# Kernel tuning notes

Measured on AMD Instinct MI355X. Metric: run time of the kernel, lower is better.

Reference implementation:

```python
import math
import jax, jax.numpy as jnp
import numpy as np

B, S, D, H, FF, N, V, C = 32, 512, 512, 8, 2048, 6, 32000, 16
EPS = 1e-6


def setup_inputs() -> dict:
    key = jax.random.key(0)
    c = [0]
    def w(shape, scale=0.02):
        c[0] += 1
        return jax.random.normal(jax.random.fold_in(key, c[0]), shape, jnp.float32) * scale
    inp = {}
    inp['src_emb'] = w((V, D)).at[0].set(0.0)  # padding_idx=0 row zeroed
    inp['tgt_emb'] = w((C, D)).at[0].set(0.0)
    for p in ['e', 'd', 's']:  # encoder self / decoder self / decoder cross attn
        for nm in ['wq', 'wk', 'wv', 'wo']:
            inp[f'{p}_{nm}'] = w((N, D, D))
            inp[f'{p}_{nm.replace("w", "b")}'] = w((N, D))
    for p in ['e', 'd']:
        inp[f'{p}_w1'] = w((N, D, FF)); inp[f'{p}_b1'] = w((N, FF))
        inp[f'{p}_w2'] = w((N, FF, D)); inp[f'{p}_b2'] = w((N, D))
    inp['gen_w'] = w((D * C, C)); inp['gen_b'] = w((C,))
    inp['scr_x'] = jax.random.randint(jax.random.fold_in(key, 999), (B, S), 0, V, dtype=jnp.int32)
    return inp


def _layernorm(x):
    # torch source: (x - mean) / (std + eps), std is unbiased (ddof=1); gamma=1, beta=0
    m = x.mean(-1, keepdims=True)
    s = jnp.std(x, axis=-1, keepdims=True, ddof=1)
    return (x - m) / (s + EPS)


def _mha(xq, xkv, wq, bq, wk, bk, wv, bv, wo, bo):
    b, lq, _ = xq.shape
    lk = xkv.shape[1]
    dk = D // H
    q = (xq @ wq + bq).reshape(b, lq, H, dk)
    k = (xkv @ wk + bk).reshape(b, lk, H, dk)
    v = (xkv @ wv + bv).reshape(b, lk, H, dk)
    scores = jnp.einsum('bqhd,bkhd->bhqk', q, k) / math.sqrt(dk)
    p = jax.nn.softmax(scores, axis=-1)
    o = jnp.einsum('bhqk,bkhd->bqhd', p, v).reshape(b, lq, D)
    return o @ wo + bo


def _ffn(x, w1, b1, w2, b2):
    return jax.nn.relu(x @ w1 + b1) @ w2 + b2


def _pos_encoding(L):
    pos = jnp.arange(L, dtype=jnp.float32)[:, None]
    div = jnp.exp(jnp.arange(0, D, 2, dtype=jnp.float32) * (-math.log(10000.0) / D))
    pe = jnp.zeros((L, D), jnp.float32)
    pe = pe.at[:, 0::2].set(jnp.sin(pos * div))
    pe = pe.at[:, 1::2].set(jnp.cos(pos * div))
    return pe


def reference(src_emb, tgt_emb,
              e_wq, e_bq, e_wk, e_bk, e_wv, e_bv, e_wo, e_bo, e_w1, e_b1, e_w2, e_b2,
              d_wq, d_bq, d_wk, d_bk, d_wv, d_bv, d_wo, d_bo,
              s_wq, s_bq, s_wk, s_bk, s_wv, s_bv, s_wo, s_bo,
              d_w1, d_b1, d_w2, d_b2, gen_w, gen_b, scr_x):
    sqrt_d = math.sqrt(D)
    # encoder
    x = src_emb[scr_x] * sqrt_d + _pos_encoding(S)[None]
    for i in range(N):
        t = _layernorm(x)
        x = x + _mha(t, t, e_wq[i], e_bq[i], e_wk[i], e_bk[i], e_wv[i], e_bv[i], e_wo[i], e_bo[i])
        t = _layernorm(x)
        x = x + _ffn(t, e_w1[i], e_b1[i], e_w2[i], e_b2[i])
    enc = _layernorm(x)
    # decoder over classify targets arange(C), repeated over batch
    y = jnp.broadcast_to(tgt_emb * sqrt_d + _pos_encoding(C), (B, C, D))
    for i in range(N):
        t = _layernorm(y)
        y = y + _mha(t, t, d_wq[i], d_bq[i], d_wk[i], d_bk[i], d_wv[i], d_bv[i], d_wo[i], d_bo[i])
        t = _layernorm(y)
        y = y + _mha(t, enc, s_wq[i], s_bq[i], s_wk[i], s_bk[i], s_wv[i], s_bv[i], s_wo[i], s_bo[i])
        t = _layernorm(y)
        y = y + _ffn(t, d_w1[i], d_b1[i], d_w2[i], d_b2[i])
    dec = _layernorm(y)
    logits = dec.reshape(B, -1) @ gen_w + gen_b
    return jax.nn.log_softmax(logits, axis=-1)
```

## Files before the change

kernel.cpp:

```cpp
#include <hip/hip_runtime.h>
#include <math.h>

#define NB  32
#define SS  512
#define DD  512
#define HH  8
#define FFD 2048
#define NLAY 6
#define CC  16
#define SQRTD 22.627416997969522f

typedef unsigned short u16;
typedef __attribute__((ext_vector_type(8))) short short8;
typedef __attribute__((ext_vector_type(8))) unsigned short u16x8;
typedef __attribute__((ext_vector_type(4))) float f32x4;

__device__ __forceinline__ u16 f2bf(float f) {
  unsigned u = __builtin_bit_cast(unsigned, f);
  u += 0x7fff + ((u >> 16) & 1);
  return (u16)(u >> 16);
}
__device__ __forceinline__ float bf2f(u16 u) {
  unsigned v = ((unsigned)u) << 16;
  return __builtin_bit_cast(float, v);
}
__device__ __forceinline__ void async16(const u16* g, u16* l) {
  __builtin_amdgcn_global_load_lds(
      (const __attribute__((address_space(1))) unsigned int*)g,
      (__attribute__((address_space(3))) unsigned int*)l, 16, 0, 0);
}
__device__ __forceinline__ int swz(int row, int slice) {
  return row * 128 + ((slice ^ (row & 7)) << 4);
}
__device__ __forceinline__ int vswz(int row, int slice) {
  return row * 128 + ((slice ^ (row & 7) ^ ((row >> 4) & 3)) << 4);
}

__device__ __forceinline__ float pe_val(int pos, int d) {
  int j = d >> 1;
  float freq = expf((float)j * -0.03597789207f);
  float ang = (float)pos * freq;
  return (d & 1) ? cosf(ang) : sinf(ang);
}

__global__ __launch_bounds__(512) void k_embed_src(
    const float* __restrict__ emb, const int* __restrict__ ids,
    float* __restrict__ x) {
  int tok = blockIdx.x;
  int d = threadIdx.x;
  int s = tok & (SS - 1);
  int id = ids[tok];
  x[(size_t)tok * DD + d] = emb[(size_t)id * DD + d] * SQRTD + pe_val(s, d);
}

__global__ __launch_bounds__(512) void k_embed_tgt(
    const float* __restrict__ emb, float* __restrict__ y) {
  int tok = blockIdx.x;
  int d = threadIdx.x;
  int c = tok & (CC - 1);
  y[(size_t)tok * DD + d] = emb[(size_t)c * DD + d] * SQRTD + pe_val(c, d);
}

template <typename OT>
__global__ __launch_bounds__(256) void k_layernorm(
    const float* __restrict__ X, OT* __restrict__ Y) {
  int row = blockIdx.x;
  int tid = threadIdx.x;
  int lane = tid & 63, wv = tid >> 6;
  const float* x = X + (size_t)row * DD;
  float2 v = *(const float2*)(x + tid * 2);
  float s = v.x + v.y;
  #pragma unroll
  for (int off = 32; off; off >>= 1) s += __shfl_xor(s, off);
  __shared__ float red[4];
  if (lane == 0) red[wv] = s;
  __syncthreads();
  float mean = (red[0] + red[1] + red[2] + red[3]) * (1.0f / DD);
  float dx = v.x - mean, dy = v.y - mean;
  float sq = dx * dx + dy * dy;
  #pragma unroll
  for (int off = 32; off; off >>= 1) sq += __shfl_xor(sq, off);
  __syncthreads();
  if (lane == 0) red[wv] = sq;
  __syncthreads();
  float var = (red[0] + red[1] + red[2] + red[3]) * (1.0f / (DD - 1));
  float inv = 1.0f / (sqrtf(var) + 1e-6f);
  float ox = dx * inv, oy = dy * inv;
  if constexpr (sizeof(OT) == 2) {
    ushort2 o; o.x = f2bf(ox); o.y = f2bf(oy);
    *(ushort2*)((u16*)Y + (size_t)row * DD + tid * 2) = o;
  } else {
    float2 o; o.x = ox; o.y = oy;
    *(float2*)((float*)Y + (size_t)row * DD + tid * 2) = o;
  }
}

__global__ __launch_bounds__(256) void k_wt(
    const float* __restrict__ in, u16* __restrict__ out, int K, int N,
    size_t ldl, int roff) {
  __shared__ float tile[32][33];
  const float* ip = in + (size_t)blockIdx.z * K * N;
  u16* op = out + (size_t)blockIdx.z * ldl;
  int n0 = blockIdx.x * 32, k0 = blockIdx.y * 32;
  int tx = threadIdx.x, ty = threadIdx.y;
  #pragma unroll
  for (int i = 0; i < 32; i += 8)
    tile[ty + i][tx] = ip[(size_t)(k0 + ty + i) * N + n0 + tx];
  __syncthreads();
  #pragma unroll
  for (int i = 0; i < 32; i += 8)
    op[(size_t)(roff + n0 + ty + i) * K + k0 + tx] = f2bf(tile[tx][ty + i]);
}

__global__ void k_bcat(const float* __restrict__ b0, const float* __restrict__ b1,
                       const float* __restrict__ b2, float* __restrict__ out,
                       int n0, int n1, int n2) {
  int lay = blockIdx.x, nt = n0 + n1 + n2;
  for (int t = threadIdx.x; t < nt; t += blockDim.x) {
    float v;
    if (t < n0) v = b0[(size_t)lay * n0 + t];
    else if (t < n0 + n1) v = b1[(size_t)lay * n1 + t - n0];
    else v = b2[(size_t)lay * n2 + t - n0 - n1];
    out[(size_t)lay * nt + t] = v;
  }
}

template <typename OT, bool RELU, bool RES, int NT>
__global__ __launch_bounds__(256) void k_mgemm(
    const u16* __restrict__ A, const u16* __restrict__ Bt,
    const float* __restrict__ bias, const float* __restrict__ res,
    OT* __restrict__ C, int M, int N, int K) {
  constexpr int MI = (NT == 128) ? 4 : 2;
  __shared__ u16 As[2][128 * 32];
  __shared__ u16 Bs[2][NT * 32];
  int nbn = N / NT;
  int cpx = gridDim.x >> 3;
  int bid = (blockIdx.x & 7) * cpx + (blockIdx.x >> 3);
  int bm = bid / nbn, bn = bid % nbn;
  int tid = threadIdx.x;
  int wid = tid >> 6, lane = tid & 63;
  int i0 = 2 * wid, i1 = 2 * wid + 1;
  int r0 = 16 * i0 + (lane >> 2), r1 = 16 * i1 + (lane >> 2);
  int kof = (lane & 3) * 8;
  const u16* Ag0 = A + (size_t)(bm * 128 + r0) * K + kof;
  const u16* Ag1 = A + (size_t)(bm * 128 + r1) * K + kof;
  const u16* Bg0;
  const u16* Bg1 = nullptr;
  if constexpr (NT == 128) {
    Bg0 = Bt + (size_t)(bn * 128 + r0) * K + kof;
    Bg1 = Bt + (size_t)(bn * 128 + r1) * K + kof;
  } else {
    int rb = 16 * wid + (lane >> 2);
    Bg0 = Bt + (size_t)(bn * 64 + rb) * K + kof;
  }
  f32x4 acc[MI][4] = {};
  int wm = wid >> 1, wn = wid & 1;
  int aoff, boff;
  if constexpr (NT == 128) {
    aoff = (wm * 64 + (lane & 15)) * 32 + (lane >> 4) * 8;
    boff = (wn * 64 + (lane & 15)) * 32 + (lane >> 4) * 8;
  } else {
    aoff = (wid * 32 + (lane & 15)) * 32 + (lane >> 4) * 8;
    boff = (lane & 15) * 32 + (lane >> 4) * 8;
  }

  auto stage = [&](int buf, int kel) {
    async16(Ag0 + kel, &As[buf][i0 * 512]);
    async16(Ag1 + kel, &As[buf][i1 * 512]);
    if constexpr (NT == 128) {
      async16(Bg0 + kel, &Bs[buf][i0 * 512]);
      async16(Bg1 + kel, &Bs[buf][i1 * 512]);
    } else {
      async16(Bg0 + kel, &Bs[buf][wid * 512]);
    }
  };

  stage(0, 0);
  __syncthreads();
  int nkt = K >> 5;
  for (int kt = 0; kt < nkt; ++kt) {
    int cur = kt & 1;
    if (kt + 1 < nkt) stage(cur ^ 1, (kt + 1) << 5);
    short8 af[MI], bfr[4];
    #pragma unroll
    for (int i = 0; i < MI; ++i)
      af[i] = *(const short8*)&As[cur][aoff + i * 16 * 32];
    #pragma unroll
    for (int i = 0; i < 4; ++i)
      bfr[i] = *(const short8*)&Bs[cur][boff + i * 16 * 32];
    #pragma unroll
    for (int mi = 0; mi < MI; ++mi)
      #pragma unroll
      for (int ni = 0; ni < 4; ++ni)
        acc[mi][ni] = __builtin_amdgcn_mfma_f32_16x16x32_bf16(
            af[mi], bfr[ni], acc[mi][ni], 0, 0, 0);
    __syncthreads();
  }

  int colb, rowb;
  if constexpr (NT == 128) {
    colb = bn * 128 + wn * 64 + (lane & 15);
    rowb = bm * 128 + wm * 64 + ((lane >> 4) << 2);
  } else {
    colb = bn * 64 + (lane & 15);
    rowb = bm * 128 + wid * 32 + ((lane >> 4) << 2);
  }
  #pragma unroll
  for (int mi = 0; mi < MI; ++mi)
    #pragma unroll
    for (int ni = 0; ni < 4; ++ni) {
      int col = colb + ni * 16;
      float bv = bias[col];
      #pragma unroll
      for (int r = 0; r < 4; ++r) {
        int row = rowb + mi * 16 + r;
        float v = acc[mi][ni][r] + bv;
        if constexpr (RES) v += res[(size_t)row * N + col];
        if constexpr (RELU) v = fmaxf(v, 0.f);
        if constexpr (sizeof(OT) == 2) ((u16*)C)[(size_t)row * N + col] = f2bf(v);
        else ((float*)C)[(size_t)row * N + col] = v;
      }
    }
}

__global__ __launch_bounds__(256) void k_attn3(
    const u16* __restrict__ Q, const u16* __restrict__ K,
    const u16* __restrict__ V, u16* __restrict__ O,
    int Lq, int Lk, int nqt, int ldq, int ldk, int ldv, int ldo) {
  __shared__ u16 Qs[64 * 64];
  __shared__ u16 Ks[64 * 64];
  __shared__ u16 VsT[64 * 64];
  __shared__ u16 Ps[64 * 64];
  int cpx = gridDim.x >> 3;
  int bid = (blockIdx.x & 7) * cpx + (blockIdx.x >> 3);
  int qt = bid % nqt;
  int bh = bid / nqt;
  int b = bh >> 3, h = bh & 7;
  int tid = threadIdx.x;
  int wv = tid >> 6, lane = tid & 63;
  int l16 = lane & 15, l4 = lane >> 4;
  int sr = tid >> 2;
  int sc2 = (tid & 3) << 1;

  {
    int qr = qt * 64 + sr;
    const u16* g = Q + (size_t)((size_t)b * Lq + qr) * ldq + h * 64 + (sc2 << 3);
    u16x8 v0 = *(const u16x8*)g;
    u16x8 v1 = *(const u16x8*)(g + 8);
    *(u16x8*)((char*)Qs + swz(sr, sc2)) = v0;
    *(u16x8*)((char*)Qs + swz(sr, sc2 + 1)) = v1;
  }

  f32x4 o_acc[4] = {};
  float l_r[4] = {0.f, 0.f, 0.f, 0.f};
  int qrow = wv * 16 + l16;

  int nkt = Lk >> 6;
  for (int kt = 0; kt < nkt; ++kt) {
    __syncthreads();
    {
      int kr = kt * 64 + sr;
      const u16* gk = K + (size_t)((size_t)b * Lk + kr) * ldk + h * 64 + (sc2 << 3);
      const u16* gv = V + (size_t)((size_t)b * Lk + kr) * ldv + h * 64 + (sc2 << 3);
      u16x8 k0 = *(const u16x8*)gk;
      u16x8 k1 = *(const u16x8*)(gk + 8);
      u16x8 vv0 = *(const u16x8*)gv;
      u16x8 vv1 = *(const u16x8*)(gv + 8);
      *(u16x8*)((char*)Ks + swz(sr, sc2)) = k0;
      *(u16x8*)((char*)Ks + swz(sr, sc2 + 1)) = k1;
      bool oddr = sr & 1;
      u16x8 send = oddr ? vv0 : vv1;
      int4 si = __builtin_bit_cast(int4, send);
      int4 ri;
      ri.x = __shfl_xor(si.x, 4); ri.y = __shfl_xor(si.y, 4);
      ri.z = __shfl_xor(si.z, 4); ri.w = __shfl_xor(si.w, 4);
      u16x8 recv = __builtin_bit_cast(u16x8, ri);
      int colbyte = (sr & 6) << 1;
      int slice = sr >> 3;
      int dbase = (sc2 << 3) + (oddr ? 8 : 0);
      #pragma unroll
      for (int j = 0; j < 8; ++j) {
        u16 lo = oddr ? recv[j] : vv0[j];
        u16 hi = oddr ? vv1[j] : recv[j];
        *(unsigned*)((char*)VsT + vswz(dbase + j, slice) + colbyte) =
            (unsigned)lo | ((unsigned)hi << 16);
      }
    }
    __syncthreads();

    short8 aQ0 = *(const short8*)((char*)Qs + swz(qrow, l4));
    short8 aQ1 = *(const short8*)((char*)Qs + swz(qrow, 4 + l4));
    f32x4 s_acc[4];
    #pragma unroll
    for (int ni = 0; ni < 4; ++ni) {
      int krow = ni * 16 + l16;
      short8 b0 = *(const short8*)((char*)Ks + swz(krow, l4));
      short8 b1 = *(const short8*)((char*)Ks + swz(krow, 4 + l4));
      f32x4 z = {};
      z = __builtin_amdgcn_mfma_f32_16x16x32_bf16(aQ0, b0, z, 0, 0, 0);
      z = __builtin_amdgcn_mfma_f32_16x16x32_bf16(aQ1, b1, z, 0, 0, 0);
      s_acc[ni] = z;
    }

    #pragma unroll
    for (int r = 0; r < 4; ++r) {
      int prow = wv * 16 + l4 * 4 + r;
      #pragma unroll
      for (int ni = 0; ni < 4; ++ni) {
        float p = __expf(s_acc[ni][r] * 0.125f);
        l_r[r] += p;
        int e = ni * 16 + l16;
        ((u16*)((char*)Ps + swz(prow, e >> 3)))[e & 7] = f2bf(p);
      }
    }

    short8 aP0 = *(const short8*)((char*)Ps + swz(qrow, l4));
    short8 aP1 = *(const short8*)((char*)Ps + swz(qrow, 4 + l4));
    #pragma unroll
    for (int ni = 0; ni < 4; ++ni) {
      int vrow = ni * 16 + l16;
      short8 b0 = *(const short8*)((char*)VsT + vswz(vrow, l4));
      short8 b1 = *(const short8*)((char*)VsT + vswz(vrow, 4 + l4));
      o_acc[ni] = __builtin_amdgcn_mfma_f32_16x16x32_bf16(aP0, b0, o_acc[ni], 0, 0, 0);
      o_acc[ni] = __builtin_amdgcn_mfma_f32_16x16x32_bf16(aP1, b1, o_acc[ni], 0, 0, 0);
    }
  }

  #pragma unroll
  for (int r = 0; r < 4; ++r)
    #pragma unroll
    for (int off = 8; off; off >>= 1) l_r[r] += __shfl_xor(l_r[r], off);

  #pragma unroll
  for (int r = 0; r < 4; ++r) {
    int q = qt * 64 + wv * 16 + l4 * 4 + r;
    float inv = 1.0f / l_r[r];
    u16* op = O + (size_t)((size_t)b * Lq + q) * ldo + h * 64 + l16;
    #pragma unroll
    for (int ni = 0; ni < 4; ++ni)
      op[ni * 16] = f2bf(o_acc[ni][r] * inv);
  }
}

__global__ __launch_bounds__(256) void k_attn4(
    const u16* __restrict__ Q, const u16* __restrict__ K,
    const u16* __restrict__ V, u16* __restrict__ O,
    int Lk, int ldq, int ldk, int ldv, int ldo) {
  __shared__ u16 Qs[16 * 64];
  __shared__ u16 Ks[4][64 * 64];
  __shared__ u16 VsT[4][64 * 64];
  __shared__ u16 Ps[4][16 * 64];
  int cpx = gridDim.x >> 3;
  int bid = (blockIdx.x & 7) * cpx + (blockIdx.x >> 3);
  int b = bid >> 3, h = bid & 7;
  int tid = threadIdx.x;
  int wv = tid >> 6, lane = tid & 63;
  int l16 = lane & 15, l4 = lane >> 4;

  if (tid < 64) {
    int qr = tid >> 2;
    int sc2 = (tid & 3) << 1;
    const u16* g = Q + (size_t)((size_t)b * CC + qr) * ldq + h * 64 + (sc2 << 3);
    u16x8 v0 = *(const u16x8*)g;
    u16x8 v1 = *(const u16x8*)(g + 8);
    *(u16x8*)((char*)Qs + swz(qr, sc2)) = v0;
    *(u16x8*)((char*)Qs + swz(qr, sc2 + 1)) = v1;
  }
  __syncthreads();

  u16* KsW = Ks[wv];
  u16* VsW = VsT[wv];
  u16* PsW = Ps[wv];

  f32x4 o_acc[4] = {};
  float l_r[4] = {0.f, 0.f, 0.f, 0.f};

  int nkt = (Lk + 63) >> 6;
  for (int kt = wv; kt < nkt; kt += 4) {
    int kr = kt * 64 + lane; if (kr >= Lk) kr = Lk - 1;
    const u16* gk = K + (size_t)((size_t)b * Lk + kr) * ldk + h * 64;
    const u16* gv = V + (size_t)((size_t)b * Lk + kr) * ldv + h * 64;
    u16x8 vvv[8];
    #pragma unroll
    for (int c = 0; c < 8; ++c) {
      u16x8 kk = *(const u16x8*)(gk + c * 8);
      *(u16x8*)((char*)KsW + swz(lane, c)) = kk;
      vvv[c] = *(const u16x8*)(gv + c * 8);
    }
    bool oddr = lane & 1;
    int4 s0 = __builtin_bit_cast(int4, oddr ? vvv[0] : vvv[4]);
    int4 s1 = __builtin_bit_cast(int4, oddr ? vvv[1] : vvv[5]);
    int4 s2 = __builtin_bit_cast(int4, oddr ? vvv[2] : vvv[6]);
    int4 s3 = __builtin_bit_cast(int4, oddr ? vvv[3] : vvv[7]);
    int4 r0, r1, r2, r3;
    r0.x = __shfl_xor(s0.x, 1); r0.y = __shfl_xor(s0.y, 1);
    r0.z = __shfl_xor(s0.z, 1); r0.w = __shfl_xor(s0.w, 1);
    r1.x = __shfl_xor(s1.x, 1); r1.y = __shfl_xor(s1.y, 1);
    r1.z = __shfl_xor(s1.z, 1); r1.w = __shfl_xor(s1.w, 1);
    r2.x = __shfl_xor(s2.x, 1); r2.y = __shfl_xor(s2.y, 1);
    r2.z = __shfl_xor(s2.z, 1); r2.w = __shfl_xor(s2.w, 1);
    r3.x = __shfl_xor(s3.x, 1); r3.y = __shfl_xor(s3.y, 1);
    r3.z = __shfl_xor(s3.z, 1); r3.w = __shfl_xor(s3.w, 1);
    u16x8 rcv[4] = {
      __builtin_bit_cast(u16x8, r0), __builtin_bit_cast(u16x8, r1),
      __builtin_bit_cast(u16x8, r2), __builtin_bit_cast(u16x8, r3)};
    int colbyte = (lane & 6) << 1;
    int slice = lane >> 3;
    int dbase = oddr ? 32 : 0;
    #pragma unroll
    for (int c = 0; c < 4; ++c)
      #pragma unroll
      for (int j = 0; j < 8; ++j) {
        int d = dbase + c * 8 + j;
        u16 lo = oddr ? rcv[c][j] : vvv[c][j];
        u16 hi = oddr ? vvv[4 + c][j] : rcv[c][j];
        *(unsigned*)((char*)VsW + vswz(d, slice) + colbyte) =
            (unsigned)lo | ((unsigned)hi << 16);
      }

    short8 aQ0 = *(const short8*)((char*)Qs + swz(l16, l4));
    short8 aQ1 = *(const short8*)((char*)Qs + swz(l16, 4 + l4));
    f32x4 s_acc[4];
    #pragma unroll
    for (int ni = 0; ni < 4; ++ni) {
      int krow = ni * 16 + l16;
      short8 b0 = *(const short8*)((char*)KsW + swz(krow, l4));
      short8 b1 = *(const short8*)((char*)KsW + swz(krow, 4 + l4));
      f32x4 z = {};
      z = __builtin_amdgcn_mfma_f32_16x16x32_bf16(aQ0, b0, z, 0, 0, 0);
      z = __builtin_amdgcn_mfma_f32_16x16x32_bf16(aQ1, b1, z, 0, 0, 0);
      s_acc[ni] = z;
    }

    #pragma unroll
    for (int r = 0; r < 4; ++r) {
      int prow = l4 * 4 + r;
      #pragma unroll
      for (int ni = 0; ni < 4; ++ni) {
        int kg = kt * 64 + ni * 16 + l16;
        float p = (kg < Lk) ? __expf(s_acc[ni][r] * 0.125f) : 0.f;
        l_r[r] += p;
        int e = ni * 16 + l16;
        ((u16*)((char*)PsW + swz(prow, e >> 3)))[e & 7] = f2bf(p);
      }
    }

    short8 aP0 = *(const short8*)((char*)PsW + swz(l16, l4));
    short8 aP1 = *(const short8*)((char*)PsW + swz(l16, 4 + l4));
    #pragma unroll
    for (int ni = 0; ni < 4; ++ni) {
      int vrow = ni * 16 + l16;
      short8 b0 = *(const short8*)((char*)VsW + vswz(vrow, l4));
      short8 b1 = *(const short8*)((char*)VsW + vswz(vrow, 4 + l4));
      o_acc[ni] = __builtin_amdgcn_mfma_f32_16x16x32_bf16(aP0, b0, o_acc[ni], 0, 0, 0);
      o_acc[ni] = __builtin_amdgcn_mfma_f32_16x16x32_bf16(aP1, b1, o_acc[ni], 0, 0, 0);
    }
  }

  #pragma unroll
  for (int r = 0; r < 4; ++r)
    #pragma unroll
    for (int off = 8; off; off >>= 1) l_r[r] += __shfl_xor(l_r[r], off);

  float* cO = (float*)KsW;
  float* cL = (float*)VsW;
  #pragma unroll
  for (int r = 0; r < 4; ++r) {
    int q = l4 * 4 + r;
    if (l16 == 0) cL[q] = l_r[r];
    #pragma unroll
    for (int ni = 0; ni < 4; ++ni)
      cO[q * 64 + ni * 16 + l16] = o_acc[ni][r];
  }
  __syncthreads();

  #pragma unroll
  for (int i = 0; i < 4; ++i) {
    int e = tid + 256 * i;
    int q = e >> 6, d = e & 63;
    float den = 0.f, num = 0.f;
    #pragma unroll
    for (int w = 0; w < 4; ++w) {
      den += ((float*)VsT[w])[q];
      num += ((float*)Ks[w])[q * 64 + d];
    }
    O[(size_t)((size_t)b * CC + q) * ldo + h * 64 + d] = f2bf(num / den);
  }
}

__global__ __launch_bounds__(256) void k_gen(
    const float* __restrict__ dec, const float* __restrict__ Wg,
    const float* __restrict__ bg, float* __restrict__ out) {
  int b = blockIdx.x;
  int t = threadIdx.x;
  int n = t & 15, ch = t >> 4;
  const float* a = dec + (size_t)b * (CC * DD);
  float p = 0.f;
  int k0 = ch * 512;
  for (int kk = k0; kk < k0 + 512; ++kk) p += a[kk] * Wg[(size_t)kk * CC + n];
  __shared__ float red[16][17];
  red[ch][n] = p;
  __syncthreads();
  __shared__ float ls[16];
  __shared__ float mm[2];
  if (t < 16) {
    float sv = bg[t];
    #pragma unroll
    for (int jj = 0; jj < 16; ++jj) sv += red[jj][t];
    ls[t] = sv;
  }
  __syncthreads();
  if (t == 0) {
    float m = ls[0];
    for (int jj = 1; jj < 16; ++jj) m = fmaxf(m, ls[jj]);
    float se = 0.f;
    for (int jj = 0; jj < 16; ++jj) se += expf(ls[jj] - m);
    mm[0] = m; mm[1] = logf(se);
  }
  __syncthreads();
  if (t < 16) out[(size_t)b * CC + t] = ls[t] - mm[0] - mm[1];
}

extern "C" void kernel_launch(void* const* d_in, const int* in_sizes, int n_in,
                              void* d_out, int out_size, void* d_ws, size_t ws_size,
                              hipStream_t stream) {
  (void)in_sizes; (void)n_in; (void)out_size; (void)ws_size;
  const float* src_emb = (const float*)d_in[0];
  const float* tgt_emb = (const float*)d_in[1];
  const float* e_wq = (const float*)d_in[2];
  const float* e_bq = (const float*)d_in[3];
  const float* e_wk = (const float*)d_in[4];
  const float* e_bk = (const float*)d_in[5];
  const float* e_wv = (const float*)d_in[6];
  const float* e_bv = (const float*)d_in[7];
  const float* e_wo = (const float*)d_in[8];
  const float* e_bo = (const float*)d_in[9];
  const float* d_wq = (const float*)d_in[10];
  const float* d_bq = (const float*)d_in[11];
  const float* d_wk = (const float*)d_in[12];
  const float* d_bk = (const float*)d_in[13];
  const float* d_wv = (const float*)d_in[14];
  const float* d_bv = (const float*)d_in[15];
  const float* d_wo = (const float*)d_in[16];
  const float* d_bo = (const float*)d_in[17];
  const float* s_wq = (const float*)d_in[18];
  const float* s_bq = (const float*)d_in[19];
  const float* s_wk = (const float*)d_in[20];
  const float* s_bk = (const float*)d_in[21];
  const float* s_wv = (const float*)d_in[22];
  const float* s_bv = (const float*)d_in[23];
  const float* s_wo = (const float*)d_in[24];
  const float* s_bo = (const float*)d_in[25];
  const float* e_w1 = (const float*)d_in[26];
  const float* e_b1 = (const float*)d_in[27];
  const float* e_w2 = (const float*)d_in[28];
  const float* e_b2 = (const float*)d_in[29];
  const float* dw1  = (const float*)d_in[30];
  const float* db1  = (const float*)d_in[31];
  const float* dw2  = (const float*)d_in[32];
  const float* db2  = (const float*)d_in[33];
  const float* gen_w = (const float*)d_in[34];
  const float* gen_b = (const float*)d_in[35];
  const int*   scr   = (const int*)d_in[36];

  float* ws = (float*)d_ws;
  const size_t NBS = (size_t)NB * SS * DD;
  const size_t BCD = (size_t)NB * CC * DD;
  float* x    = ws;
  u16*  t_bf  = (u16*)(ws + NBS);
  u16*  enc_bf = t_bf;
  float* dsm  = ws + NBS + NBS / 2;
  float* dy   = dsm;
  float* tdf  = dsm + BCD;
  u16*  td_bf = (u16*)(tdf + BCD);
  u16*  aod_bf = td_bf + BCD;
  u16*  dqkv_act = aod_bf + BCD;
  u16*  middd_bf = dqkv_act + 3 * BCD;
  u16*  eqkv_act = (u16*)(ws + 2 * NBS);
  u16*  midd_e   = eqkv_act;
  u16*  kv_big   = eqkv_act;
  u16*  kv_x     = (u16*)x;
  u16* wp = (u16*)(ws + 4 * NBS);
  const size_t SQKV = (size_t)NLAY * 1536 * 512;
  const size_t SDD  = (size_t)NLAY * 512 * 512;
  const size_t SKV  = (size_t)NLAY * 1024 * 512;
  const size_t SFF  = (size_t)NLAY * 2048 * 512;
  u16* eqkv_t = wp;            wp += SQKV;
  u16* ewo_t  = wp;            wp += SDD;
  u16* ew1_t  = wp;            wp += SFF;
  u16* ew2_t  = wp;            wp += SFF;
  u16* dqkv_t = wp;            wp += SQKV;
  u16* dwo_t  = wp;            wp += SDD;
  u16* sq_t   = wp;            wp += SDD;
  u16* skv_t  = wp;            wp += SKV;
  u16* swo_t  = wp;            wp += SDD;
  u16* dw1_t  = wp;            wp += SFF;
  u16* dw2_t  = wp;            wp += SFF;
  float* ebqkv = (float*)wp;
  float* dbqkv = ebqkv + NLAY * 1536;
  float* sbkv  = dbqkv + NLAY * 1536;

  const int BS = NB * SS;
  const int BC = NB * CC;

  auto wt = [&](const float* in, u16* out, int K, int N, size_t ldl, int roff) {
    k_wt<<<dim3(N / 32, K / 32, NLAY), dim3(32, 8), 0, stream>>>(in, out, K, N, ldl, roff);
  };
  auto mg = [&](const u16* A, const u16* Bt, const float* bias,
                const float* res, void* C, int M, int N, int K, int relu, int obf) {
    int g128 = (M / 128) * (N / 128);
    if (g128 >= 1024) {
      dim3 g(g128);
      if (obf) {
        if (relu) k_mgemm<u16, true, false, 128><<<g, 256, 0, stream>>>(A, Bt, bias, nullptr, (u16*)C, M, N, K);
        else      k_mgemm<u16, false, false, 128><<<g, 256, 0, stream>>>(A, Bt, bias, nullptr, (u16*)C, M, N, K);
      } else {
        if (res)  k_mgemm<float, false, true, 128><<<g, 256, 0, stream>>>(A, Bt, bias, res, (float*)C, M, N, K);
        else      k_mgemm<float, false, false, 128><<<g, 256, 0, stream>>>(A, Bt, bias, nullptr, (float*)C, M, N, K);
      }
    } else {
      dim3 g((M / 128) * (N / 64));
      if (obf) {
        if (relu) k_mgemm<u16, true, false, 64><<<g, 256, 0, stream>>>(A, Bt, bias, nullptr, (u16*)C, M, N, K);
        else      k_mgemm<u16, false, false, 64><<<g, 256, 0, stream>>>(A, Bt, bias, nullptr, (u16*)C, M, N, K);
      } else {
        if (res)  k_mgemm<float, false, true, 64><<<g, 256, 0, stream>>>(A, Bt, bias, res, (float*)C, M, N, K);
        else      k_mgemm<float, false, false, 64><<<g, 256, 0, stream>>>(A, Bt, bias, nullptr, (float*)C, M, N, K);
      }
    }
  };

  wt(e_wq, eqkv_t, 512, 512, 1536 * 512, 0);
  wt(e_wk, eqkv_t, 512, 512, 1536 * 512, 512);
  wt(e_wv, eqkv_t, 512, 512, 1536 * 512, 1024);
  wt(e_wo, ewo_t,  512, 512, 512 * 512, 0);
  wt(e_w1, ew1_t,  512, 2048, 2048 * 512, 0);
  wt(e_w2, ew2_t,  2048, 512, (size_t)512 * 2048, 0);
  wt(d_wq, dqkv_t, 512, 512, 1536 * 512, 0);
  wt(d_wk, dqkv_t, 512, 512, 1536 * 512, 512);
  wt(d_wv, dqkv_t, 512, 512, 1536 * 512, 1024);
  wt(d_wo, dwo_t,  512, 512, 512 * 512, 0);
  wt(s_wq, sq_t,   512, 512, 512 * 512, 0);
  wt(s_wk, skv_t,  512, 512, 1024 * 512, 0);
  wt(s_wv, skv_t,  512, 512, 1024 * 512, 512);
  wt(s_wo, swo_t,  512, 512, 512 * 512, 0);
  wt(dw1,  dw1_t,  512, 2048, 2048 * 512, 0);
  wt(dw2,  dw2_t,  2048, 512, (size_t)512 * 2048, 0);
  k_bcat<<<NLAY, 512, 0, stream>>>(e_bq, e_bk, e_bv, ebqkv, 512, 512, 512);
  k_bcat<<<NLAY, 512, 0, stream>>>(d_bq, d_bk, d_bv, dbqkv, 512, 512, 512);
  k_bcat<<<NLAY, 512, 0, stream>>>(s_bk, s_bv, s_bv, sbkv, 512, 512, 0);

  k_embed_src<<<BS, 512, 0, stream>>>(src_emb, scr, x);
  for (int i = 0; i < NLAY; ++i) {
    size_t bo = (size_t)i * DD, b1o = (size_t)i * FFD;
    k_layernorm<u16><<<BS, 256, 0, stream>>>(x, t_bf);
    mg(t_bf, eqkv_t + (size_t)i * 1536 * 512, ebqkv + i * 1536, nullptr,
       eqkv_act, BS, 1536, 512, 0, 1);
    k_attn3<<<NB * HH * (SS / 64), 256, 0, stream>>>(
        eqkv_act, eqkv_act + 512, eqkv_act + 1024, t_bf,
        SS, SS, SS / 64, 1536, 1536, 1536, 512);
    mg(t_bf, ewo_t + (size_t)i * 512 * 512, e_bo + bo, x, x, BS, 512, 512, 0, 0);
    k_layernorm<u16><<<BS, 256, 0, stream>>>(x, t_bf);
    mg(t_bf, ew1_t + (size_t)i * 2048 * 512, e_b1 + b1o, nullptr,
       midd_e, BS, 2048, 512, 1, 1);
    mg(midd_e, ew2_t + (size_t)i * 512 * 2048, e_b2 + bo, x, x, BS, 512, 2048, 0, 0);
  }
  k_layernorm<u16><<<BS, 256, 0, stream>>>(x, enc_bf);

  mg(enc_bf, skv_t, sbkv, nullptr, kv_big, BS, 2048, 512, 0, 1);
  mg(enc_bf, skv_t + (size_t)2 * 1024 * 512, sbkv + 2 * 1024, nullptr,
     kv_x, BS, 1024, 512, 0, 1);

  k_embed_tgt<<<BC, 512, 0, stream>>>(tgt_emb, dy);
  for (int i = 0; i < NLAY; ++i) {
    size_t bo = (size_t)i * DD, b1o = (size_t)i * FFD;
    if (i == 2)
      mg(enc_bf, skv_t + (size_t)3 * 1024 * 512, sbkv + 3 * 1024, nullptr,
         kv_big, BS, 2048, 512, 0, 1);
    if (i == 3)
      mg(enc_bf, skv_t + (size_t)5 * 1024 * 512, sbkv + 5 * 1024, nullptr,
         kv_x, BS, 1024, 512, 0, 1);
    k_layernorm<u16><<<BC, 256, 0, stream>>>(dy, td_bf);
    mg(td_bf, dqkv_t + (size_t)i * 1536 * 512, dbqkv + i * 1536, nullptr,
       dqkv_act, BC, 1536, 512, 0, 1);
    k_attn4<<<NB * HH, 256, 0, stream>>>(
        dqkv_act, dqkv_act + 512, dqkv_act + 1024, aod_bf,
        CC, 1536, 1536, 1536, 512);
    mg(aod_bf, dwo_t + (size_t)i * 512 * 512, d_bo + bo, dy, dy, BC, 512, 512, 0, 0);
    k_layernorm<u16><<<BC, 256, 0, stream>>>(dy, td_bf);
    mg(td_bf, sq_t + (size_t)i * 512 * 512, s_bq + bo, nullptr,
       dqkv_act, BC, 512, 512, 0, 1);
    const u16* kvp; int ldkv;
    if (i < 2)      { kvp = kv_big + i * 1024;        ldkv = 2048; }
    else if (i == 2){ kvp = kv_x;                     ldkv = 1024; }
    else if (i < 5) { kvp = kv_big + (i - 3) * 1024;  ldkv = 2048; }
    else            { kvp = kv_x;                     ldkv = 1024; }
    k_attn4<<<NB * HH, 256, 0, stream>>>(
        dqkv_act, kvp, kvp + 512, aod_bf,
        SS, 512, ldkv, ldkv, 512);
    mg(aod_bf, swo_t + (size_t)i * 512 * 512, s_bo + bo, dy, dy, BC, 512, 512, 0, 0);
    k_layernorm<u16><<<BC, 256, 0, stream>>>(dy, td_bf);
    mg(td_bf, dw1_t + (size_t)i * 2048 * 512, db1 + b1o, nullptr,
       middd_bf, BC, 2048, 512, 1, 1);
    mg(middd_bf, dw2_t + (size_t)i * 512 * 2048, db2 + bo, dy, dy, BC, 512, 2048, 0, 0);
  }
  k_layernorm<float><<<BC, 256, 0, stream>>>(dy, tdf);
  k_gen<<<NB, 256, 0, stream>>>(tdf, gen_w, gen_b, (float*)d_out);
}
```

Measured before the change: 2.436 ms.

## Deepen NT=64 GEMM pipeline to four LDS buffers with explicit vmcnt waits

For the NT=64 GEMM variant, shared memory grows to four stages, and each iteration prefetches two K-tiles ahead while computing two. Loads are waited on with explicit s_waitcnt vmcnt plus raw s_barrier instead of __syncthreads after every tile. The aim is to hide global-load latency and halve the barrier count. This uses more LDS and depends on the hand-coded vmcnt count matching the number of outstanding async loads per stage.

```diff
diff --git a/kernel.cpp b/kernel.cpp
--- a/kernel.cpp
+++ b/kernel.cpp
@@ -131,8 +131,9 @@
     const float* __restrict__ bias, const float* __restrict__ res,
     OT* __restrict__ C, int M, int N, int K) {
   constexpr int MI = (NT == 128) ? 4 : 2;
-  __shared__ u16 As[2][128 * 32];
-  __shared__ u16 Bs[2][NT * 32];
+  constexpr int NBUF = (NT == 128) ? 2 : 4;
+  __shared__ u16 As[NBUF][128 * 32];
+  __shared__ u16 Bs[NBUF][NT * 32];
   int nbn = N / NT;
   int cpx = gridDim.x >> 3;
   int bid = (blockIdx.x & 7) * cpx + (blockIdx.x >> 3);
@@ -174,27 +175,54 @@
       async16(Bg0 + kel, &Bs[buf][wid * 512]);
     }
   };
-
-  stage(0, 0);
-  __syncthreads();
-  int nkt = K >> 5;
-  for (int kt = 0; kt < nkt; ++kt) {
-    int cur = kt & 1;
-    if (kt + 1 < nkt) stage(cur ^ 1, (kt + 1) << 5);
+  auto compute = [&](int buf) {
     short8 af[MI], bfr[4];
     #pragma unroll
     for (int i = 0; i < MI; ++i)
-      af[i] = *(const short8*)&As[cur][aoff + i * 16 * 32];
+      af[i] = *(const short8*)&As[buf][aoff + i * 16 * 32];
     #pragma unroll
     for (int i = 0; i < 4; ++i)
-      bfr[i] = *(const short8*)&Bs[cur][boff + i * 16 * 32];
+      bfr[i] = *(const short8*)&Bs[buf][boff + i * 16 * 32];
     #pragma unroll
     for (int mi = 0; mi < MI; ++mi)
       #pragma unroll
       for (int ni = 0; ni < 4; ++ni)
         acc[mi][ni] = __builtin_amdgcn_mfma_f32_16x16x32_bf16(
             af[mi], bfr[ni], acc[mi][ni], 0, 0, 0);
+  };
+
+  int nkt = K >> 5;
+  if constexpr (NT == 128) {
+    stage(0, 0);
     __syncthreads();
+    for (int kt = 0; kt < nkt; ++kt) {
+      int cur = kt & 1;
+      if (kt + 1 < nkt) stage(cur ^ 1, (kt + 1) << 5);
+      compute(cur);
+      __syncthreads();
+    }
+  } else {
+    stage(0, 0);
+    stage(1, 32);
+    int nit = nkt >> 1;
+    int base = 0;
+    for (int j = 0; j < nit; ++j) {
+      if (j + 1 < nit) {
+        int ob = base ^ 2;
+        stage(ob, (2 * j + 2) << 5);
+        stage(ob + 1, (2 * j + 3) << 5);
+        asm volatile("s_waitcnt vmcnt(6)" ::: "memory");
+      } else {
+        asm volatile("s_waitcnt vmcnt(0)" ::: "memory");
+      }
+      __builtin_amdgcn_s_barrier();
+      __builtin_amdgcn_sched_barrier(0);
+      compute(base);
+      compute(base + 1);
+      __builtin_amdgcn_s_barrier();
+      __builtin_amdgcn_sched_barrier(0);
+      base ^= 2;
+    }
   }
 
   int colb, rowb;
```

After: 2.418 ms. Within noise of the previous version (-0.7%).
